# Kernel tuning notes

Hardware: AMD Instinct MI355X
Metric: run time of the kernel (lower is better)

The kernel has to match this reference:

```python
import jax, jax.numpy as jnp
import numpy as np

B, C = 2000000, 24

def setup_inputs() -> dict:
    key = jax.random.key(0)
    k1, k2 = jax.random.split(key)
    input = jax.random.normal(k1, (B, C), dtype=jnp.float32)
    target = jax.random.randint(k2, (B, C), 0, 2, dtype=jnp.int32)
    return {"input": input, "target": target}

def reference(input, target):
    # LSEP: loss = log1p( sum_i sum_{p in pos_i, n in neg_i} exp(x_in - x_ip) ) / B
    # The ragged double loop factorizes per row:
    #   sum_{p,n} exp(x_n - x_p) = (sum_n exp(x_n)) * (sum_p exp(-x_p))
    pos = target > 0
    neg = target == 0
    s_neg = jnp.sum(jnp.where(neg, jnp.exp(input), 0.0), axis=1)   # [B]
    s_pos = jnp.sum(jnp.where(pos, jnp.exp(-input), 0.0), axis=1)  # [B]
    total = jnp.sum(s_neg * s_pos)
    batch_size = input.shape[0]
    return jnp.log1p(total) / batch_size
```

## Files before the change

kernel.cpp:

```cpp
#include <hip/hip_runtime.h>
#include <math.h>


constexpr int  ROWS  = 2000000;
constexpr int  BLOCK = 256;
constexpr int  GRID  = 2048;
constexpr int  TILE  = 256;
constexpr int  NT    = (ROWS + TILE - 1) / TILE;
constexpr long TOT4  = (long)ROWS * 6;

__global__ __launch_bounds__(BLOCK) void lsep_main(
        const float4* __restrict__ input,
        const int4*   __restrict__ target,
        double*       __restrict__ partials)
{
    __shared__ float  lds_a[TILE * 7];
    __shared__ float  lds_b[TILE * 7];
    __shared__ double sred[BLOCK / 64];

    const int t = threadIdx.x;
    double acc = 0.0;

    for (int tile = blockIdx.x; tile < NT; tile += GRID) {
        const long base4 = (long)tile * (TILE * 6);

        float4 x[6]; int4 tg[6]; bool ok[6];
        #pragma unroll
        for (int k = 0; k < 6; ++k) {
            const long g4 = base4 + t + k * BLOCK;
            ok[k] = (g4 < TOT4);
            if (ok[k]) { x[k] = input[g4]; tg[k] = target[g4]; }
        }

        #pragma unroll
        for (int k = 0; k < 6; ++k) {
            if (ok[k]) {
                float a = 0.0f, b = 0.0f, e;
                e = __expf(tg[k].x > 0 ? -x[k].x : x[k].x); if (tg[k].x > 0) b += e; else a += e;
                e = __expf(tg[k].y > 0 ? -x[k].y : x[k].y); if (tg[k].y > 0) b += e; else a += e;
                e = __expf(tg[k].z > 0 ? -x[k].z : x[k].z); if (tg[k].z > 0) b += e; else a += e;
                e = __expf(tg[k].w > 0 ? -x[k].w : x[k].w); if (tg[k].w > 0) b += e; else a += e;
                const int lr  = t + k * BLOCK;
                const int row = lr / 6;
                const int j   = lr - row * 6;
                lds_a[row * 7 + j] = a;
                lds_b[row * 7 + j] = b;
            }
        }
        __syncthreads();

        const long grow = (long)tile * TILE + t;
        if (grow < ROWS) {
            const int r7 = t * 7;
            const float sa = ((lds_a[r7+0] + lds_a[r7+1]) + (lds_a[r7+2] + lds_a[r7+3]))
                           +  (lds_a[r7+4] + lds_a[r7+5]);
            const float sb = ((lds_b[r7+0] + lds_b[r7+1]) + (lds_b[r7+2] + lds_b[r7+3]))
                           +  (lds_b[r7+4] + lds_b[r7+5]);
            acc += (double)sa * (double)sb;
        }
        __syncthreads();
    }

    #pragma unroll
    for (int off = 32; off > 0; off >>= 1)
        acc += __shfl_down(acc, off, 64);
    if ((t & 63) == 0) sred[t >> 6] = acc;
    __syncthreads();
    if (t == 0)
        partials[blockIdx.x] = (sred[0] + sred[1]) + (sred[2] + sred[3]);
}

__global__ void lsep_finalize(const double* __restrict__ partials,
                              float* __restrict__ out)
{
    __shared__ double sred[4];
    const int t = threadIdx.x;
    double s = 0.0;
    #pragma unroll
    for (int i = 0; i < GRID / 256; ++i) s += partials[t + i * 256];
    #pragma unroll
    for (int off = 32; off > 0; off >>= 1)
        s += __shfl_down(s, off, 64);
    if ((t & 63) == 0) sred[t >> 6] = s;
    __syncthreads();
    if (t == 0)
        out[0] = (float)(log1p((sred[0] + sred[1]) + (sred[2] + sred[3])) / (double)ROWS);
}

extern "C" void kernel_launch(void* const* d_in, const int* in_sizes, int n_in,
                              void* d_out, int out_size, void* d_ws, size_t ws_size,
                              hipStream_t stream) {
    const float4* input  = (const float4*)d_in[0];
    const int4*   target = (const int4*)d_in[1];
    double*       ws     = (double*)d_ws;
    float*        out    = (float*)d_out;

    lsep_main<<<GRID, BLOCK, 0, stream>>>(input, target, ws);
    lsep_finalize<<<1, 256, 0, stream>>>(ws, out);
}
```

Baseline: 381.1 us.

## Replace LDS row transpose with half-row-per-thread loads and shuffle pairing

Each thread now handles half a row, 12 contiguous elements loaded as three float4/int4, and combines with its neighbour lane through a shuffle xor. This removes the shared-memory staging and both per-tile barriers. The grid is sized so that work divides exactly with no bounds checks, and the next iteration's loads are software-prefetched into registers. Both lanes of a pair add the same product, so the finalize step halves the total. Each thread now reads three consecutive 16-byte vectors, a strided rather than fully coalesced pattern, and the prefetch raises register pressure.

```diff
diff --git a/kernel.cpp b/kernel.cpp
--- a/kernel.cpp
+++ b/kernel.cpp
@@ -2,68 +2,62 @@
 #include <math.h>
 
 
-constexpr int  ROWS  = 2000000;
-constexpr int  BLOCK = 256;
-constexpr int  GRID  = 2048;
-constexpr int  TILE  = 256;
-constexpr int  NT    = (ROWS + TILE - 1) / TILE;
-constexpr long TOT4  = (long)ROWS * 6;
+constexpr int  ROWS    = 2000000;
+constexpr int  HALVES  = ROWS * 2;
+constexpr int  BLOCK   = 256;
+constexpr int  GRID    = 3125;
+constexpr int  THREADS = GRID * BLOCK;
+constexpr int  ITERS   = HALVES / THREADS;
 
-__global__ __launch_bounds__(BLOCK) void lsep_main(
+__global__ __launch_bounds__(BLOCK, 4) void lsep_main(
         const float4* __restrict__ input,
         const int4*   __restrict__ target,
         double*       __restrict__ partials)
 {
-    __shared__ float  lds_a[TILE * 7];
-    __shared__ float  lds_b[TILE * 7];
-    __shared__ double sred[BLOCK / 64];
+    const int tid = blockIdx.x * BLOCK + threadIdx.x;
 
-    const int t = threadIdx.x;
     double acc = 0.0;
 
-    for (int tile = blockIdx.x; tile < NT; tile += GRID) {
-        const long base4 = (long)tile * (TILE * 6);
+    float4 xa0, xa1, xa2; int4 ta0, ta1, ta2;
+    {
+        const int f = 3 * tid;
+        xa0 = input[f];  xa1 = input[f + 1];  xa2 = input[f + 2];
+        ta0 = target[f]; ta1 = target[f + 1]; ta2 = target[f + 2];
+    }
 
-        float4 x[6]; int4 tg[6]; bool ok[6];
-        #pragma unroll
-        for (int k = 0; k < 6; ++k) {
-            const long g4 = base4 + t + k * BLOCK;
-            ok[k] = (g4 < TOT4);
-            if (ok[k]) { x[k] = input[g4]; tg[k] = target[g4]; }
+    int h = tid;
+    #pragma unroll
+    for (int i = 0; i < ITERS; ++i) {
+        float4 xb0, xb1, xb2; int4 tb0, tb1, tb2;
+        if (i + 1 < ITERS) {
+            const int f = 3 * (h + THREADS);
+            xb0 = input[f];  xb1 = input[f + 1];  xb2 = input[f + 2];
+            tb0 = target[f]; tb1 = target[f + 1]; tb2 = target[f + 2];
         }
 
-        #pragma unroll
-        for (int k = 0; k < 6; ++k) {
-            if (ok[k]) {
-                float a = 0.0f, b = 0.0f, e;
-                e = __expf(tg[k].x > 0 ? -x[k].x : x[k].x); if (tg[k].x > 0) b += e; else a += e;
-                e = __expf(tg[k].y > 0 ? -x[k].y : x[k].y); if (tg[k].y > 0) b += e; else a += e;
-                e = __expf(tg[k].z > 0 ? -x[k].z : x[k].z); if (tg[k].z > 0) b += e; else a += e;
-                e = __expf(tg[k].w > 0 ? -x[k].w : x[k].w); if (tg[k].w > 0) b += e; else a += e;
-                const int lr  = t + k * BLOCK;
-                const int row = lr / 6;
-                const int j   = lr - row * 6;
-                lds_a[row * 7 + j] = a;
-                lds_b[row * 7 + j] = b;
-            }
-        }
-        __syncthreads();
+        float a = 0.0f, b = 0.0f, e;
+        #define LSEP_ELEM(xc, tc) \
+            e = __expf(tc > 0 ? -xc : xc); \
+            if (tc > 0) b += e; else a += e;
+        LSEP_ELEM(xa0.x, ta0.x) LSEP_ELEM(xa0.y, ta0.y) LSEP_ELEM(xa0.z, ta0.z) LSEP_ELEM(xa0.w, ta0.w)
+        LSEP_ELEM(xa1.x, ta1.x) LSEP_ELEM(xa1.y, ta1.y) LSEP_ELEM(xa1.z, ta1.z) LSEP_ELEM(xa1.w, ta1.w)
+        LSEP_ELEM(xa2.x, ta2.x) LSEP_ELEM(xa2.y, ta2.y) LSEP_ELEM(xa2.z, ta2.z) LSEP_ELEM(xa2.w, ta2.w)
+        #undef LSEP_ELEM
 
-        const long grow = (long)tile * TILE + t;
-        if (grow < ROWS) {
-            const int r7 = t * 7;
-            const float sa = ((lds_a[r7+0] + lds_a[r7+1]) + (lds_a[r7+2] + lds_a[r7+3]))
-                           +  (lds_a[r7+4] + lds_a[r7+5]);
-            const float sb = ((lds_b[r7+0] + lds_b[r7+1]) + (lds_b[r7+2] + lds_b[r7+3]))
-                           +  (lds_b[r7+4] + lds_b[r7+5]);
-            acc += (double)sa * (double)sb;
-        }
-        __syncthreads();
+        const float sa = a + __shfl_xor(a, 1, 64);
+        const float sb = b + __shfl_xor(b, 1, 64);
+        acc += (double)sa * (double)sb;
+
+        xa0 = xb0; xa1 = xb1; xa2 = xb2;
+        ta0 = tb0; ta1 = tb1; ta2 = tb2;
+        h += THREADS;
     }
 
+    __shared__ double sred[BLOCK / 64];
     #pragma unroll
     for (int off = 32; off > 0; off >>= 1)
         acc += __shfl_down(acc, off, 64);
+    const int t = threadIdx.x;
     if ((t & 63) == 0) sred[t >> 6] = acc;
     __syncthreads();
     if (t == 0)
@@ -76,15 +70,16 @@
     __shared__ double sred[4];
     const int t = threadIdx.x;
     double s = 0.0;
-    #pragma unroll
-    for (int i = 0; i < GRID / 256; ++i) s += partials[t + i * 256];
+    for (int i = t; i < GRID; i += 256) s += partials[i];
     #pragma unroll
     for (int off = 32; off > 0; off >>= 1)
         s += __shfl_down(s, off, 64);
     if ((t & 63) == 0) sred[t >> 6] = s;
     __syncthreads();
-    if (t == 0)
-        out[0] = (float)(log1p((sred[0] + sred[1]) + (sred[2] + sred[3])) / (double)ROWS);
+    if (t == 0) {
+        const double total = ((sred[0] + sred[1]) + (sred[2] + sred[3])) * 0.5;
+        out[0] = (float)(log1p(total) / (double)ROWS);
+    }
 }
 
 extern "C" void kernel_launch(void* const* d_in, const int* in_sizes, int n_in,
```

Measured after the change: 377.4 us. No clear change (-1.0%).
